# Performance work log

Measured on AMD Instinct MI355X. Metric: run time of the kernel, lower is better.

Reference implementation:

```python
import jax, jax.numpy as jnp
import numpy as np

V = 100000   # num_items
D = 128      # embedding_dim
B = 2048     # sessions per batch
S = 8        # nodes per session
N = B * S    # total nodes
E = B * (S - 1)  # chain edges per session
SCALE = 12.0


def setup_inputs() -> dict:
    key = jax.random.key(0)
    ks = jax.random.split(key, 16)
    stdv = 1.0 / np.sqrt(D)  # NISER.reset_parameters: uniform(-stdv, stdv)
    u = lambda k, shp: jax.random.uniform(k, shp, jnp.float32, -stdv, stdv)
    iid = jax.random.randint(ks[0], (N,), 0, V)
    node_seg = jnp.repeat(jnp.arange(B), S)            # node -> session id
    last_nodes = jnp.arange(B) * S + (S - 1)           # last node per session
    base = jnp.arange(N).reshape(B, S)
    src = base[:, :-1].reshape(-1)                     # chain edges i -> i+1
    dst = base[:, 1:].reshape(-1)
    w = jax.random.uniform(ks[1], (E,), jnp.float32, 0.1, 1.0)
    return dict(
        iid=iid, src=src, dst=dst, node_seg=node_seg, last_nodes=last_nodes, w=w,
        emb=u(ks[2], (V, D)),
        W1=u(ks[3], (D, D)), W2=u(ks[4], (D, D)),
        W_ih=u(ks[5], (3 * D, 2 * D)), W_hh=u(ks[6], (3 * D, D)),
        b_ih=u(ks[7], (3 * D,)), b_hh=u(ks[8], (3 * D,)),
        Wu=u(ks[9], (D, 2 * D)), Wv=u(ks[10], (D, 2 * D)), bv=u(ks[11], (D,)),
        We=u(ks[12], (1, D)), Wout=u(ks[13], (D, 2 * D)),
        Wsr=u(ks[14], (D, 3 * D)))


def _norm(x, eps):
    return x / (jnp.linalg.norm(x, axis=-1, keepdims=True) + eps)


def _gru_cell(x, h, W_ih, W_hh, b_ih, b_hh):
    # torch.nn.GRUCell semantics
    gi = x @ W_ih.T + b_ih
    gh = h @ W_hh.T + b_hh
    i_r, i_z, i_n = jnp.split(gi, 3, axis=-1)
    h_r, h_z, h_n = jnp.split(gh, 3, axis=-1)
    r = jax.nn.sigmoid(i_r + h_r)
    z = jax.nn.sigmoid(i_z + h_z)
    n = jnp.tanh(i_n + r * h_n)
    return (1.0 - z) * n + z * h


def _neigh(feat, s, d, w, n_nodes):
    # weighted mean of incoming messages: sum(ft[src]*w) / sum(w) per dst node
    m = jax.ops.segment_sum(feat[s] * w[:, None], d, num_segments=n_nodes)
    ws = jax.ops.segment_sum(w, d, num_segments=n_nodes)
    return m / jnp.where(ws == 0, 1.0, ws)[:, None]  # zero-degree nodes -> 0


def reference(iid, src, dst, node_seg, last_nodes, w, emb,
              W1, W2, W_ih, W_hh, b_ih, b_hh,
              Wu, Wv, bv, We, Wout, Wsr):
    n_nodes = iid.shape[0]
    n_seg = last_nodes.shape[0]
    feat = _norm(emb[iid], 1e-12)                       # [N, D], L2-normalized
    # --- SRGNN layer (forward + reverse message passing, GRU fuse) ---
    n1 = _neigh(feat, src, dst, w, n_nodes) @ W1.T
    n2 = _neigh(feat, dst, src, w, n_nodes) @ W2.T      # reverse graph
    out = _gru_cell(jnp.concatenate([n1, n2], axis=-1), feat, W_ih, W_hh, b_ih, b_hh)
    feat = jnp.concatenate([out, feat], axis=-1)        # [N, 2D]
    feat = feat / jnp.linalg.norm(feat, axis=-1, keepdims=True)  # no eps, as source
    # --- AttnReadout: segment softmax attention pooling ---
    fu = feat @ Wu.T                                    # [N, D]
    fv = feat[last_nodes] @ Wv.T + bv                   # [B, D]
    e = jax.nn.sigmoid(fu + fv[node_seg]) @ We.T        # [N, 1]
    emax = jax.ops.segment_max(e, node_seg, num_segments=n_seg)
    ee = jnp.exp(e - emax[node_seg])
    alpha = ee / jax.ops.segment_sum(ee, node_seg, num_segments=n_seg)[node_seg]
    sr_g = jax.ops.segment_sum(feat * alpha, node_seg, num_segments=n_seg) @ Wout.T
    # --- session representation + scaled log-softmax over items ---
    sr_l = feat[last_nodes]                             # [B, 2D]
    sr = jnp.concatenate([sr_l, sr_g], axis=-1) @ Wsr.T # [B, D]
    sr = _norm(sr, 1e-12)
    target = _norm(emb, 1e-12)                          # [V, D]
    logits = sr @ target.T                              # [B, V]
    return jax.nn.log_softmax(SCALE * logits, axis=-1)
```

## Files before the change

kernel.cpp:

```cpp
#include <hip/hip_runtime.h>
#include <hip/hip_bf16.h>

#define D 128
#define NV 100000
#define NB 2048
#define SS 8
#define NN (NB*SS)
#define NE (NB*(SS-1))
#define VPAD 100096
#define CBLK 782
#define LSCALE 12.0f

typedef __attribute__((ext_vector_type(4))) float f32x4;
typedef __attribute__((ext_vector_type(8))) short bf16x8;

__device__ inline float warp_sum64(float v){
  #pragma unroll
  for (int off=1; off<64; off<<=1) v += __shfl_xor(v, off, 64);
  return v;
}

__global__ void k_feat(const int* __restrict__ iid, const float* __restrict__ emb,
                       float* __restrict__ feat){
  int node = blockIdx.x*4 + (threadIdx.x>>6);
  int l = threadIdx.x & 63;
  int idx = iid[node];
  float v0 = emb[(size_t)idx*D + l];
  float v1 = emb[(size_t)idx*D + 64 + l];
  float ss = warp_sum64(v0*v0 + v1*v1);
  float inv = 1.0f/(sqrtf(ss)+1e-12f);
  feat[node*D + l]      = v0*inv;
  feat[node*D + 64 + l] = v1*inv;
}

__global__ void k_scatter(const int* __restrict__ src, const int* __restrict__ dst,
                          const float* __restrict__ w, const float* __restrict__ feat,
                          float* __restrict__ m1, float* __restrict__ m2,
                          float* __restrict__ ws1, float* __restrict__ ws2){
  int e = blockIdx.x*2 + (threadIdx.x>>7);
  int d = threadIdx.x & 127;
  int s = src[e], dd = dst[e];
  float wt = w[e];
  atomicAdd(&m1[dd*D + d], feat[s*D + d]*wt);
  atomicAdd(&m2[s*D + d],  feat[dd*D + d]*wt);
  if (d==0){ atomicAdd(&ws1[dd], wt); atomicAdd(&ws2[s], wt); }
}

__global__ void k_neighdiv(float* __restrict__ m1, float* __restrict__ m2,
                           const float* __restrict__ ws1, const float* __restrict__ ws2){
  int i = blockIdx.x*256 + threadIdx.x;
  int n = i >> 7;
  float a = ws1[n], b = ws2[n];
  m1[i] = a>0.f ? m1[i]/a : 0.f;
  m2[i] = b>0.f ? m2[i]/b : 0.f;
}

__global__ __launch_bounds__(256) void gemm_bt(
    const float* __restrict__ A, int lda,
    const float* __restrict__ W,
    const float* __restrict__ bias,
    float* __restrict__ C, int ldc, int K)
{
  __shared__ float As[16][65];
  __shared__ float Ws[16][65];
  int tid = threadIdx.x;
  int tx = tid & 15, ty = tid >> 4;
  int row0 = blockIdx.y*64, col0 = blockIdx.x*64;
  int r = tid >> 2, c4 = (tid & 3)*4;
  float acc[4][4] = {};
  for (int k0=0;k0<K;k0+=16){
    float4 a  = *(const float4*)&A[(size_t)(row0+r)*lda + k0 + c4];
    float4 wv = *(const float4*)&W[(size_t)(col0+r)*K  + k0 + c4];
    As[c4+0][r]=a.x;  As[c4+1][r]=a.y;  As[c4+2][r]=a.z;  As[c4+3][r]=a.w;
    Ws[c4+0][r]=wv.x; Ws[c4+1][r]=wv.y; Ws[c4+2][r]=wv.z; Ws[c4+3][r]=wv.w;
    __syncthreads();
    #pragma unroll
    for (int kk=0;kk<16;kk++){
      float ar[4], wr[4];
      #pragma unroll
      for (int i=0;i<4;i++) ar[i]=As[kk][ty*4+i];
      #pragma unroll
      for (int j=0;j<4;j++) wr[j]=Ws[kk][tx*4+j];
      #pragma unroll
      for (int i=0;i<4;i++)
        #pragma unroll
        for (int j=0;j<4;j++) acc[i][j] += ar[i]*wr[j];
    }
    __syncthreads();
  }
  #pragma unroll
  for (int i=0;i<4;i++){
    int rr = row0+ty*4+i;
    #pragma unroll
    for (int j=0;j<4;j++){
      int cc = col0+tx*4+j;
      float v = acc[i][j] + (bias ? bias[cc] : 0.f);
      C[(size_t)rr*ldc + cc] = v;
    }
  }
}

__global__ void k_gru(const float* __restrict__ gi, const float* __restrict__ gh,
                      const float* __restrict__ feat, float* __restrict__ feat2){
  int node = blockIdx.x*4 + (threadIdx.x>>6);
  int l = threadIdx.x & 63;
  float o[2], f[2];
  float ss = 0.f;
  #pragma unroll
  for (int h=0;h<2;h++){
    int d = l + h*64;
    float ir = gi[node*384 + d], iz = gi[node*384 + 128 + d], in_ = gi[node*384 + 256 + d];
    float hr = gh[node*384 + d], hz = gh[node*384 + 128 + d], hn  = gh[node*384 + 256 + d];
    float rg = 1.f/(1.f+__expf(-(ir+hr)));
    float zg = 1.f/(1.f+__expf(-(iz+hz)));
    float ng = tanhf(in_ + rg*hn);
    float fd = feat[node*D + d];
    float od = (1.f-zg)*ng + zg*fd;
    o[h]=od; f[h]=fd;
    ss += od*od + fd*fd;
  }
  ss = warp_sum64(ss);
  float inv = 1.f/sqrtf(ss);
  feat2[node*256 + l]       = o[0]*inv;
  feat2[node*256 + 64 + l]  = o[1]*inv;
  feat2[node*256 + 128 + l] = f[0]*inv;
  feat2[node*256 + 192 + l] = f[1]*inv;
}

__global__ void k_gather(const int* __restrict__ last_nodes, const float* __restrict__ feat2,
                         float* __restrict__ srcat){
  int b = blockIdx.x, d = threadIdx.x;
  srcat[b*384 + d] = feat2[last_nodes[b]*256 + d];
}

__global__ void k_escore(const float* __restrict__ fu, const float* __restrict__ fv,
                         const int* __restrict__ node_seg, const float* __restrict__ We,
                         float* __restrict__ evec){
  int node = blockIdx.x*4 + (threadIdx.x>>6);
  int l = threadIdx.x & 63;
  int seg = node_seg[node];
  float s = 0.f;
  #pragma unroll
  for (int h=0;h<2;h++){
    int d = l + h*64;
    float x = fu[node*D + d] + fv[seg*D + d];
    s += (1.f/(1.f+__expf(-x))) * We[d];
  }
  s = warp_sum64(s);
  if (l==0) evec[node]=s;
}

__global__ void k_attnpool(const float* __restrict__ evec, const float* __restrict__ feat2,
                           float* __restrict__ sg){
  __shared__ float ev[SS];
  int b = blockIdx.x, t = threadIdx.x;
  if (t < SS) ev[t] = evec[b*SS + t];
  __syncthreads();
  float m = ev[0];
  #pragma unroll
  for (int s=1;s<SS;s++) m = fmaxf(m, ev[s]);
  float al[SS]; float se = 0.f;
  #pragma unroll
  for (int s=0;s<SS;s++){ al[s] = __expf(ev[s]-m); se += al[s]; }
  float inv = 1.f/se;
  float acc = 0.f;
  #pragma unroll
  for (int s=0;s<SS;s++) acc += feat2[(b*SS+s)*256 + t] * (al[s]*inv);
  sg[b*256 + t] = acc;
}

__global__ void k_srnorm(const float* __restrict__ srb, __hip_bfloat16* __restrict__ srbf){
  int b = blockIdx.x*4 + (threadIdx.x>>6);
  int l = threadIdx.x & 63;
  float v0 = srb[b*D + l], v1 = srb[b*D + 64 + l];
  float ss = warp_sum64(v0*v0 + v1*v1);
  float inv = 1.f/(sqrtf(ss)+1e-12f);
  srbf[b*D + l]      = __float2bfloat16(v0*inv);
  srbf[b*D + 64 + l] = __float2bfloat16(v1*inv);
}

__global__ void k_tgtnorm(const float* __restrict__ emb, __hip_bfloat16* __restrict__ tgt){
  int v = blockIdx.x*4 + (threadIdx.x>>6);
  int l = threadIdx.x & 63;
  float a=0.f, b=0.f;
  if (v < NV){ a = emb[(size_t)v*D + l]; b = emb[(size_t)v*D + 64 + l]; }
  float ss = warp_sum64(a*a + b*b);
  float inv = 1.f/(sqrtf(ss)+1e-12f);
  tgt[(size_t)v*D + l]      = __float2bfloat16(a*inv);
  tgt[(size_t)v*D + 64 + l] = __float2bfloat16(b*inv);
}

__global__ __launch_bounds__(256) void k_logits(
    const __hip_bfloat16* __restrict__ Abf,
    const __hip_bfloat16* __restrict__ Bbf,
    const float* __restrict__ lse,
    float* __restrict__ psum,
    float* __restrict__ out,
    int pass)
{
  __shared__ ushort As[128][136];
  __shared__ ushort Bs[128][136];
  __shared__ float rowsum[2][128];
  int tid = threadIdx.x;
  int rowblk = blockIdx.y, colblk = blockIdx.x;
  const ushort* Au = (const ushort*)Abf;
  const ushort* Bu = (const ushort*)Bbf;
  #pragma unroll
  for (int t=0;t<8;t++){
    int c = t*256 + tid;
    int rr = c >> 4, c16 = (c & 15)*8;
    *(bf16x8*)&As[rr][c16] = *(const bf16x8*)&Au[(size_t)(rowblk*128+rr)*D + c16];
    *(bf16x8*)&Bs[rr][c16] = *(const bf16x8*)&Bu[(size_t)(colblk*128+rr)*D + c16];
  }
  __syncthreads();
  int wid = tid>>6, lane = tid&63;
  int wr = wid>>1, wc = wid&1;
  int g = lane>>4, lr = lane&15;
  f32x4 acc[4][4];
  #pragma unroll
  for (int m=0;m<4;m++)
    #pragma unroll
    for (int n=0;n<4;n++) acc[m][n] = (f32x4){0.f,0.f,0.f,0.f};
  #pragma unroll
  for (int ks=0; ks<4; ks++){
    bf16x8 af[4], bfr[4];
    #pragma unroll
    for (int m=0;m<4;m++) af[m]  = *(bf16x8*)&As[wr*64+m*16+lr][ks*32+g*8];
    #pragma unroll
    for (int n=0;n<4;n++) bfr[n] = *(bf16x8*)&Bs[wc*64+n*16+lr][ks*32+g*8];
    #pragma unroll
    for (int m=0;m<4;m++)
      #pragma unroll
      for (int n=0;n<4;n++)
        acc[m][n] = __builtin_amdgcn_mfma_f32_16x16x32_bf16(af[m], bfr[n], acc[m][n], 0,0,0);
  }
  if (pass==1){
    float s[4][4];
    #pragma unroll
    for (int m=0;m<4;m++)
      #pragma unroll
      for (int i=0;i<4;i++) s[m][i]=0.f;
    #pragma unroll
    for (int m=0;m<4;m++)
      #pragma unroll
      for (int n=0;n<4;n++){
        int col = colblk*128 + wc*64 + n*16 + lr;
        #pragma unroll
        for (int i=0;i<4;i++){
          float v = (col < NV) ? __expf(LSCALE*acc[m][n][i]) : 0.f;
          s[m][i] += v;
        }
      }
    #pragma unroll
    for (int off=1; off<16; off<<=1)
      #pragma unroll
      for (int m=0;m<4;m++)
        #pragma unroll
        for (int i=0;i<4;i++) s[m][i] += __shfl_xor(s[m][i], off, 64);
    if (lr==0){
      #pragma unroll
      for (int m=0;m<4;m++)
        #pragma unroll
        for (int i=0;i<4;i++) rowsum[wc][wr*64 + m*16 + g*4 + i] = s[m][i];
    }
    __syncthreads();
    if (tid < 128)
      psum[(size_t)colblk*NB + rowblk*128 + tid] = rowsum[0][tid] + rowsum[1][tid];
  } else {
    #pragma unroll
    for (int m=0;m<4;m++)
      #pragma unroll
      for (int i=0;i<4;i++){
        int row = rowblk*128 + wr*64 + m*16 + g*4 + i;
        float L = lse[row];
        #pragma unroll
        for (int n=0;n<4;n++){
          int col = colblk*128 + wc*64 + n*16 + lr;
          if (col < NV) out[(size_t)row*NV + col] = LSCALE*acc[m][n][i] - L;
        }
      }
  }
}

__global__ void k_lse(const float* __restrict__ psum, float* __restrict__ lse){
  int row = blockIdx.x*256 + threadIdx.x;
  float s=0.f;
  for (int cb=0;cb<CBLK;cb++) s += psum[(size_t)cb*NB + row];
  lse[row] = logf(s);
}

extern "C" void kernel_launch(void* const* d_in, const int* in_sizes, int n_in,
                              void* d_out, int out_size, void* d_ws, size_t ws_size,
                              hipStream_t stream) {
  const int*   iid        = (const int*)d_in[0];
  const int*   src        = (const int*)d_in[1];
  const int*   dst        = (const int*)d_in[2];
  const int*   node_seg   = (const int*)d_in[3];
  const int*   last_nodes = (const int*)d_in[4];
  const float* w          = (const float*)d_in[5];
  const float* emb        = (const float*)d_in[6];
  const float* W1         = (const float*)d_in[7];
  const float* W2         = (const float*)d_in[8];
  const float* W_ih       = (const float*)d_in[9];
  const float* W_hh       = (const float*)d_in[10];
  const float* b_ih       = (const float*)d_in[11];
  const float* b_hh       = (const float*)d_in[12];
  const float* Wu         = (const float*)d_in[13];
  const float* Wv         = (const float*)d_in[14];
  const float* bv         = (const float*)d_in[15];
  const float* We         = (const float*)d_in[16];
  const float* Wout       = (const float*)d_in[17];
  const float* Wsr        = (const float*)d_in[18];
  float* out = (float*)d_out;

  char* wsb = (char*)d_ws;
  size_t off = 0;
  auto alloc = [&](size_t bytes){ void* p = wsb + off; off += (bytes + 255) & ~(size_t)255; return p; };
  float* feat  = (float*)alloc((size_t)NN*D*4);
  float* m1    = (float*)alloc((size_t)NN*D*4);
  float* m2    = (float*)alloc((size_t)NN*D*4);
  float* ws1   = (float*)alloc((size_t)NN*4);
  float* ws2   = (float*)alloc((size_t)NN*4);
  float* xcat  = (float*)alloc((size_t)NN*256*4);
  float* gi    = (float*)alloc((size_t)NN*384*4);
  float* gh    = (float*)alloc((size_t)NN*384*4);
  float* feat2 = (float*)alloc((size_t)NN*256*4);
  float* fu    = (float*)alloc((size_t)NN*D*4);
  float* evec  = (float*)alloc((size_t)NN*4);
  float* srcat = (float*)alloc((size_t)NB*384*4);
  float* fv    = (float*)alloc((size_t)NB*D*4);
  float* sg    = (float*)alloc((size_t)NB*256*4);
  float* srb   = (float*)alloc((size_t)NB*D*4);
  __hip_bfloat16* srbf = (__hip_bfloat16*)alloc((size_t)NB*D*2);
  __hip_bfloat16* tgt  = (__hip_bfloat16*)alloc((size_t)VPAD*D*2);
  float* psum  = (float*)alloc((size_t)CBLK*NB*4);
  float* lse   = (float*)alloc((size_t)NB*4);

  hipMemsetAsync(m1, 0, ((size_t)2*NN*D + 2*NN)*4, stream);

  k_feat<<<NN/4, 256, 0, stream>>>(iid, emb, feat);
  k_scatter<<<NE/2, 256, 0, stream>>>(src, dst, w, feat, m1, m2, ws1, ws2);
  k_neighdiv<<<NN*D/256, 256, 0, stream>>>(m1, m2, ws1, ws2);
  gemm_bt<<<dim3(2, NN/64), 256, 0, stream>>>(m1, D, W1, nullptr, xcat, 256, D);
  gemm_bt<<<dim3(2, NN/64), 256, 0, stream>>>(m2, D, W2, nullptr, xcat+128, 256, D);
  gemm_bt<<<dim3(6, NN/64), 256, 0, stream>>>(xcat, 256, W_ih, b_ih, gi, 384, 256);
  gemm_bt<<<dim3(6, NN/64), 256, 0, stream>>>(feat, D, W_hh, b_hh, gh, 384, D);
  k_gru<<<NN/4, 256, 0, stream>>>(gi, gh, feat, feat2);
  gemm_bt<<<dim3(2, NN/64), 256, 0, stream>>>(feat2, 256, Wu, nullptr, fu, D, 256);
  k_gather<<<NB, 256, 0, stream>>>(last_nodes, feat2, srcat);
  gemm_bt<<<dim3(2, NB/64), 256, 0, stream>>>(srcat, 384, Wv, bv, fv, D, 256);
  k_escore<<<NN/4, 256, 0, stream>>>(fu, fv, node_seg, We, evec);
  k_attnpool<<<NB, 256, 0, stream>>>(evec, feat2, sg);
  gemm_bt<<<dim3(2, NB/64), 256, 0, stream>>>(sg, 256, Wout, nullptr, srcat+256, 384, 256);
  gemm_bt<<<dim3(2, NB/64), 256, 0, stream>>>(srcat, 384, Wsr, nullptr, srb, D, 384);
  k_srnorm<<<NB/4, 256, 0, stream>>>(srb, srbf);
  k_tgtnorm<<<VPAD/4, 256, 0, stream>>>(emb, tgt);
  k_logits<<<dim3(CBLK, NB/128), 256, 0, stream>>>(srbf, tgt, nullptr, psum, nullptr, 1);
  k_lse<<<NB/256, 256, 0, stream>>>(psum, lse);
  k_logits<<<dim3(CBLK, NB/128), 256, 0, stream>>>(srbf, tgt, lse, nullptr, out, 2);
}
```

Baseline: 1.446 ms.

## Fold W1/W2 into W_ih, vectorize gemm LDS reads, keep A fragments in registers

Result: no change. 1.448 ms (+0.2%).

```diff
diff --git a/kernel.cpp b/kernel.cpp
--- a/kernel.cpp
+++ b/kernel.cpp
@@ -33,26 +33,41 @@
   feat[node*D + 64 + l] = v1*inv;
 }
 
+__global__ void k_wcat(const float* __restrict__ Wih, const float* __restrict__ W1,
+                       const float* __restrict__ W2, float* __restrict__ Wcat){
+  __shared__ float wrow[256];
+  int j = blockIdx.x, k = threadIdx.x;
+  wrow[k]       = Wih[j*256 + k];
+  wrow[128 + k] = Wih[j*256 + 128 + k];
+  __syncthreads();
+  float s1 = 0.f, s2 = 0.f;
+  for (int t=0;t<128;t++){
+    s1 += wrow[t]       * W1[t*128 + k];
+    s2 += wrow[128 + t] * W2[t*128 + k];
+  }
+  Wcat[j*256 + k]       = s1;
+  Wcat[j*256 + 128 + k] = s2;
+}
+
 __global__ void k_scatter(const int* __restrict__ src, const int* __restrict__ dst,
                           const float* __restrict__ w, const float* __restrict__ feat,
-                          float* __restrict__ m1, float* __restrict__ m2,
+                          float* __restrict__ m12,
                           float* __restrict__ ws1, float* __restrict__ ws2){
   int e = blockIdx.x*2 + (threadIdx.x>>7);
   int d = threadIdx.x & 127;
   int s = src[e], dd = dst[e];
   float wt = w[e];
-  atomicAdd(&m1[dd*D + d], feat[s*D + d]*wt);
-  atomicAdd(&m2[s*D + d],  feat[dd*D + d]*wt);
+  atomicAdd(&m12[(size_t)dd*256 + d],       feat[s*D + d]*wt);
+  atomicAdd(&m12[(size_t)s*256 + 128 + d],  feat[dd*D + d]*wt);
   if (d==0){ atomicAdd(&ws1[dd], wt); atomicAdd(&ws2[s], wt); }
 }
 
-__global__ void k_neighdiv(float* __restrict__ m1, float* __restrict__ m2,
+__global__ void k_neighdiv(float* __restrict__ m12,
                            const float* __restrict__ ws1, const float* __restrict__ ws2){
   int i = blockIdx.x*256 + threadIdx.x;
-  int n = i >> 7;
-  float a = ws1[n], b = ws2[n];
-  m1[i] = a>0.f ? m1[i]/a : 0.f;
-  m2[i] = b>0.f ? m2[i]/b : 0.f;
+  int r = i >> 8, c = i & 255;
+  float s = (c < 128) ? ws1[r] : ws2[r];
+  m12[i] = s > 0.f ? m12[i]/s : 0.f;
 }
 
 __global__ __launch_bounds__(256) void gemm_bt(
@@ -61,8 +76,8 @@
     const float* __restrict__ bias,
     float* __restrict__ C, int ldc, int K)
 {
-  __shared__ float As[16][65];
-  __shared__ float Ws[16][65];
+  __shared__ float As[16][68];
+  __shared__ float Ws[16][68];
   int tid = threadIdx.x;
   int tx = tid & 15, ty = tid >> 4;
   int row0 = blockIdx.y*64, col0 = blockIdx.x*64;
@@ -76,15 +91,14 @@
     __syncthreads();
     #pragma unroll
     for (int kk=0;kk<16;kk++){
-      float ar[4], wr[4];
-      #pragma unroll
-      for (int i=0;i<4;i++) ar[i]=As[kk][ty*4+i];
-      #pragma unroll
-      for (int j=0;j<4;j++) wr[j]=Ws[kk][tx*4+j];
+      float4 ar = *(const float4*)&As[kk][ty*4];
+      float4 wr = *(const float4*)&Ws[kk][tx*4];
+      float arr[4] = {ar.x, ar.y, ar.z, ar.w};
+      float wrr[4] = {wr.x, wr.y, wr.z, wr.w};
       #pragma unroll
       for (int i=0;i<4;i++)
         #pragma unroll
-        for (int j=0;j<4;j++) acc[i][j] += ar[i]*wr[j];
+        for (int j=0;j<4;j++) acc[i][j] += arr[i]*wrr[j];
     }
     __syncthreads();
   }
@@ -198,24 +212,31 @@
     float* __restrict__ out,
     int pass)
 {
-  __shared__ ushort As[128][136];
   __shared__ ushort Bs[128][136];
   __shared__ float rowsum[2][128];
   int tid = threadIdx.x;
   int rowblk = blockIdx.y, colblk = blockIdx.x;
   const ushort* Au = (const ushort*)Abf;
   const ushort* Bu = (const ushort*)Bbf;
+  int wid = tid>>6, lane = tid&63;
+  int wr = wid>>1, wc = wid&1;
+  int g = lane>>4, lr = lane&15;
+
+  bf16x8 af[4][4];
+  #pragma unroll
+  for (int m=0;m<4;m++)
+    #pragma unroll
+    for (int ks=0;ks<4;ks++)
+      af[ks][m] = *(const bf16x8*)&Au[(size_t)(rowblk*128 + wr*64 + m*16 + lr)*D + ks*32 + g*8];
+
   #pragma unroll
   for (int t=0;t<8;t++){
     int c = t*256 + tid;
     int rr = c >> 4, c16 = (c & 15)*8;
-    *(bf16x8*)&As[rr][c16] = *(const bf16x8*)&Au[(size_t)(rowblk*128+rr)*D + c16];
     *(bf16x8*)&Bs[rr][c16] = *(const bf16x8*)&Bu[(size_t)(colblk*128+rr)*D + c16];
   }
   __syncthreads();
-  int wid = tid>>6, lane = tid&63;
-  int wr = wid>>1, wc = wid&1;
-  int g = lane>>4, lr = lane&15;
+
   f32x4 acc[4][4];
   #pragma unroll
   for (int m=0;m<4;m++)
@@ -223,16 +244,14 @@
     for (int n=0;n<4;n++) acc[m][n] = (f32x4){0.f,0.f,0.f,0.f};
   #pragma unroll
   for (int ks=0; ks<4; ks++){
-    bf16x8 af[4], bfr[4];
-    #pragma unroll
-    for (int m=0;m<4;m++) af[m]  = *(bf16x8*)&As[wr*64+m*16+lr][ks*32+g*8];
+    bf16x8 bfr[4];
     #pragma unroll
     for (int n=0;n<4;n++) bfr[n] = *(bf16x8*)&Bs[wc*64+n*16+lr][ks*32+g*8];
     #pragma unroll
     for (int m=0;m<4;m++)
       #pragma unroll
       for (int n=0;n<4;n++)
-        acc[m][n] = __builtin_amdgcn_mfma_f32_16x16x32_bf16(af[m], bfr[n], acc[m][n], 0,0,0);
+        acc[m][n] = __builtin_amdgcn_mfma_f32_16x16x32_bf16(af[ks][m], bfr[n], acc[m][n], 0,0,0);
   }
   if (pass==1){
     float s[4][4];
@@ -316,12 +335,11 @@
   char* wsb = (char*)d_ws;
   size_t off = 0;
   auto alloc = [&](size_t bytes){ void* p = wsb + off; off += (bytes + 255) & ~(size_t)255; return p; };
-  float* feat  = (float*)alloc((size_t)NN*D*4);
-  float* m1    = (float*)alloc((size_t)NN*D*4);
-  float* m2    = (float*)alloc((size_t)NN*D*4);
+  float* m12   = (float*)alloc((size_t)NN*256*4);
   float* ws1   = (float*)alloc((size_t)NN*4);
   float* ws2   = (float*)alloc((size_t)NN*4);
-  float* xcat  = (float*)alloc((size_t)NN*256*4);
+  float* feat  = (float*)alloc((size_t)NN*D*4);
+  float* Wcat  = (float*)alloc((size_t)384*256*4);
   float* gi    = (float*)alloc((size_t)NN*384*4);
   float* gh    = (float*)alloc((size_t)NN*384*4);
   float* feat2 = (float*)alloc((size_t)NN*256*4);
@@ -336,14 +354,13 @@
   float* psum  = (float*)alloc((size_t)CBLK*NB*4);
   float* lse   = (float*)alloc((size_t)NB*4);
 
-  hipMemsetAsync(m1, 0, ((size_t)2*NN*D + 2*NN)*4, stream);
+  hipMemsetAsync(m12, 0, ((size_t)NN*256 + 2*NN)*4, stream);
 
   k_feat<<<NN/4, 256, 0, stream>>>(iid, emb, feat);
-  k_scatter<<<NE/2, 256, 0, stream>>>(src, dst, w, feat, m1, m2, ws1, ws2);
-  k_neighdiv<<<NN*D/256, 256, 0, stream>>>(m1, m2, ws1, ws2);
-  gemm_bt<<<dim3(2, NN/64), 256, 0, stream>>>(m1, D, W1, nullptr, xcat, 256, D);
-  gemm_bt<<<dim3(2, NN/64), 256, 0, stream>>>(m2, D, W2, nullptr, xcat+128, 256, D);
-  gemm_bt<<<dim3(6, NN/64), 256, 0, stream>>>(xcat, 256, W_ih, b_ih, gi, 384, 256);
+  k_wcat<<<384, 128, 0, stream>>>(W_ih, W1, W2, Wcat);
+  k_scatter<<<NE/2, 256, 0, stream>>>(src, dst, w, feat, m12, ws1, ws2);
+  k_neighdiv<<<NN, 256, 0, stream>>>(m12, ws1, ws2);
+  gemm_bt<<<dim3(6, NN/64), 256, 0, stream>>>(m12, 256, Wcat, b_ih, gi, 384, 256);
   gemm_bt<<<dim3(6, NN/64), 256, 0, stream>>>(feat, D, W_hh, b_hh, gh, 384, D);
   k_gru<<<NN/4, 256, 0, stream>>>(gi, gh, feat, feat2);
   gemm_bt<<<dim3(2, NN/64), 256, 0, stream>>>(feat2, 256, Wu, nullptr, fu, D, 256);
```
